# Kernel tuning notes

Hardware: AMD Instinct MI355X
Metric: run time of the kernel (lower is better)

## Reference

```python
import jax, jax.numpy as jnp
import numpy as np

B, C, L = 32, 512, 4096
H, K = 8, 3            # heads, kernel_size
D = C // H             # head dim
G = 32                 # GroupNorm groups
PAD = (K - 1) // 2
EPS = 1e-5
NEG = -1e30


def setup_inputs() -> dict:
    key = jax.random.key(0)
    ks = jax.random.split(key, 7)
    s = 0.02
    return {
        "x": jax.random.normal(ks[0], (B, C, L), dtype=jnp.float32),
        "gamma": jnp.ones((C,), dtype=jnp.float32),
        "beta": jnp.zeros((C,), dtype=jnp.float32),
        "W_k": jax.random.normal(ks[1], (C, H * D), dtype=jnp.float32) * s,
        "W_v": jax.random.normal(ks[2], (C, H * D), dtype=jnp.float32) * s,
        "W_o": jax.random.normal(ks[3], (H * D, C), dtype=jnp.float32) * s,
        "q": jax.random.normal(ks[4], (H, D), dtype=jnp.float32) * s,     # learned queries (QnA)
        "rpe": jax.random.normal(ks[5], (H, K), dtype=jnp.float32) * s,   # relative-position bias
    }


def _group_norm(x, gamma, beta):
    # x: (B, C, L); normalize over (C//G, L) within each of G groups
    b, c, l = x.shape
    xg = x.reshape(b, G, (c // G) * l)
    mu = jnp.mean(xg, axis=-1, keepdims=True)
    var = jnp.var(xg, axis=-1, keepdims=True)
    xn = ((xg - mu) * jax.lax.rsqrt(var + EPS)).reshape(b, c, l)
    return xn * gamma[None, :, None] + beta[None, :, None]


def reference(x, gamma, beta, W_k, W_v, W_o, q, rpe):
    h = _group_norm(x, gamma, beta)                     # (B, C, L)
    ht = jnp.transpose(h, (0, 2, 1))                    # (B, L, C)
    k = (ht @ W_k).reshape(B, L, H, D)                  # (B, L, H, D)
    v = (ht @ W_v).reshape(B, L, H, D)

    scale = 1.0 / np.sqrt(D).astype(np.float32)
    logits = jnp.einsum('blhd,hd->blh', k, q) * scale   # (B, L, H)

    # sliding windows of size K (zero-padded; -inf logits at boundaries)
    lp = jnp.pad(logits, ((0, 0), (PAD, PAD), (0, 0)), constant_values=NEG)
    lwin = jnp.stack([lp[:, j:j + L] for j in range(K)], axis=2)      # (B, L, K, H)
    lwin = lwin + jnp.transpose(rpe)[None, None]                       # rpe: (H,K)->(K,H)
    attn = jax.nn.softmax(lwin, axis=2)                                # (B, L, K, H)

    vp = jnp.pad(v, ((0, 0), (PAD, PAD), (0, 0), (0, 0)))
    vwin = jnp.stack([vp[:, j:j + L] for j in range(K)], axis=2)       # (B, L, K, H, D)
    o = jnp.einsum('blkh,blkhd->blhd', attn, vwin).reshape(B, L, H * D)

    out = (o @ W_o)                                      # (B, L, C)
    return x + jnp.transpose(out, (0, 2, 1))             # residual, (B, C, L)
```

## Files before the change

kernel.cpp:

```cpp
#include <hip/hip_runtime.h>

#define Bb 32
#define Cc 512
#define Ll 4096
#define Hh 8
#define Dd 64
#define Gg 32
#define BLt (Bb * Ll)
#define NKV 520
#define NKVPAD 640

typedef __attribute__((ext_vector_type(4))) float f32x4;
typedef __attribute__((ext_vector_type(8))) short short8;
typedef __attribute__((ext_vector_type(4))) short s16x4;
typedef __attribute__((ext_vector_type(4))) int int4v;

union U16 { int4v v; short s[8]; };

__device__ __forceinline__ float bf2f(short s) {
    unsigned u = ((unsigned)(unsigned short)s) << 16;
    float f; __builtin_memcpy(&f, &u, 4); return f;
}
__device__ __forceinline__ short f2bf(float f) {
    unsigned u; __builtin_memcpy(&u, &f, 4);
    u = (u + 0x7FFFu + ((u >> 16) & 1u)) >> 16;
    return (short)u;
}

__device__ __forceinline__ int kpack(int k) {
    int blk = k >> 5, r = k & 31;
    return blk * 32 + ((r & 15) >> 2) * 8 + ((r >> 4) << 2) + (r & 3);
}

__device__ __forceinline__ int swz_off(int row, int inner) {
    return row * 128 + (inner ^ ((row & 7) << 4));
}

__device__ __forceinline__ void gload16(const short* g, short* l) {
    __builtin_amdgcn_global_load_lds((const __attribute__((address_space(1))) unsigned int*)g,
                                     (__attribute__((address_space(3))) unsigned int*)l,
                                     16, 0, 0);
}

#define BAR() __builtin_amdgcn_s_barrier()
#define SFENCE() __builtin_amdgcn_sched_barrier(0)

__global__ void k_prep(const float* __restrict__ Wk, const float* __restrict__ Wv,
                       const float* __restrict__ Wo, const float* __restrict__ q,
                       short* __restrict__ Wct, short* __restrict__ Wot, int packWo)
{
    int bid = blockIdx.x, t = threadIdx.x;
    if (bid < NKVPAD) {
        int n = bid;
        if (n < 512) {
            for (int k = t; k < 512; k += 64)
                Wct[n * 512 + kpack(k)] = f2bf(Wv[k * 512 + n]);
        } else if (n < NKV) {
            int h = n - 512;
            for (int k = t; k < 512; k += 64) {
                float acc = 0.f;
                for (int d = 0; d < 64; ++d)
                    acc += Wk[k * 512 + h * 64 + d] * q[h * 64 + d];
                Wct[n * 512 + kpack(k)] = f2bf(acc * 0.125f);
            }
        } else {
            for (int k = t; k < 512; k += 64) Wct[n * 512 + kpack(k)] = 0;
        }
    } else {
        int c = bid - NKVPAD;
        for (int k = t; k < 512; k += 64)
            Wot[c * 512 + (packWo ? kpack(k) : k)] = f2bf(Wo[k * 512 + c]);
    }
}

__global__ void k_stats(const float* __restrict__ x, float* __restrict__ stats)
{
    int bg = blockIdx.x;
    const float* p = x + (size_t)bg * 65536;
    int t = threadIdx.x;
    float s = 0.f, ss = 0.f;
    for (int i = t * 4; i < 65536; i += 1024) {
        f32x4 v = *(const f32x4*)(p + i);
        s  += v[0] + v[1] + v[2] + v[3];
        ss += v[0]*v[0] + v[1]*v[1] + v[2]*v[2] + v[3]*v[3];
    }
    for (int o = 32; o > 0; o >>= 1) { s += __shfl_down(s, o); ss += __shfl_down(ss, o); }
    __shared__ float red[8];
    int lane = t & 63, w = t >> 6;
    if (lane == 0) { red[w] = s; red[4 + w] = ss; }
    __syncthreads();
    if (t == 0) {
        float S  = red[0] + red[1] + red[2] + red[3];
        float SS = red[4] + red[5] + red[6] + red[7];
        float mean = S * (1.0f / 65536.0f);
        float var  = SS * (1.0f / 65536.0f) - mean * mean;
        stats[bg * 2]     = mean;
        stats[bg * 2 + 1] = rsqrtf(var + 1e-5f);
    }
}

__global__ void k_norm_t(const float* __restrict__ x, const float* __restrict__ gamma,
                         const float* __restrict__ beta, const float* __restrict__ stats,
                         short* __restrict__ hT)
{
    __shared__ float tile[64 * 65];
    int b = blockIdx.z, c0 = blockIdx.y * 64, l0 = blockIdx.x * 64;
    int t = threadIdx.x;
    int lq = t & 15, cq = t >> 4;
    #pragma unroll
    for (int p = 0; p < 4; ++p) {
        int cl = cq + p * 16;
        int c = c0 + cl;
        float mean = stats[(b * 32 + (c >> 4)) * 2];
        float rstd = stats[(b * 32 + (c >> 4)) * 2 + 1];
        float a  = rstd * gamma[c];
        float bb = beta[c] - mean * a;
        f32x4 v = *(const f32x4*)(x + ((size_t)b << 21) + ((size_t)c << 12) + l0 + lq * 4);
        #pragma unroll
        for (int j = 0; j < 4; ++j) tile[cl * 65 + lq * 4 + j] = v[j] * a + bb;
    }
    __syncthreads();
    int ll = t >> 2, cq4 = t & 3;
    int bl = b * Ll + l0 + ll;
    short hbuf[16];
    #pragma unroll
    for (int j = 0; j < 16; ++j) hbuf[j] = f2bf(tile[(cq4 * 16 + j) * 65 + ll]);
    short* dst = hT + (size_t)bl * 512 + ((c0 >> 5) + (cq4 >> 1)) * 32 + ((cq4 & 1) << 2);
    #pragma unroll
    for (int jj = 0; jj < 4; ++jj) {
        s16x4 v4 = { hbuf[jj*4+0], hbuf[jj*4+1], hbuf[jj*4+2], hbuf[jj*4+3] };
        *(s16x4*)(dst + jj * 8) = v4;
    }
}


template<bool PACKED>
__launch_bounds__(256, 2)
__global__ void k_gemm1(const short* __restrict__ A, const short* __restrict__ Bw,
                        short* __restrict__ vbuf, short* __restrict__ lbuf)
{
    __shared__ short sA[2][8192];
    __shared__ short sB[2][8192];
    const int t = threadIdx.x;
    const int nwg = gridDim.x * gridDim.y;
    const int bid = blockIdx.x + gridDim.x * blockIdx.y;
    const int work = (bid & 7) * (nwg >> 3) + (bid >> 3);
    const int n0 = (work % gridDim.x) * 128;
    const int m0 = (work / gridDim.x) * 128;

    const int lane = t & 63, wid = t >> 6;
    const int wm = wid >> 1, wn = wid & 1;
    const int g = lane >> 4, ln = lane & 15;

    const int srow = wid * 8 + (lane >> 3);
    const int sinner = (((lane & 7) ^ ((lane >> 3) & 7)) << 3);
    const short* gAs = A  + (size_t)(m0 + srow) * 512 + sinner;
    const short* gBs = Bw + (size_t)(n0 + srow) * 512 + sinner;

    f32x4 acc[4][4] = {};

    auto stage = [&](int kt, int buf) {
        #pragma unroll
        for (int gq = 0; gq < 4; ++gq) {
            gload16(gAs + (size_t)gq * 32 * 512 + kt * 64, &sA[buf][gq * 2048 + wid * 512]);
            gload16(gBs + (size_t)gq * 32 * 512 + kt * 64, &sB[buf][gq * 2048 + wid * 512]);
        }
    };
    auto compute = [&](int buf) {
        #pragma unroll
        for (int ks = 0; ks < 2; ++ks) {
            short8 af[4], bfr[4];
            #pragma unroll
            for (int i = 0; i < 4; ++i) {
                af[i]  = *(const short8*)((const char*)&sA[buf][0] + swz_off(wm * 64 + i * 16 + ln, ks * 64 + g * 16));
                bfr[i] = *(const short8*)((const char*)&sB[buf][0] + swz_off(wn * 64 + i * 16 + ln, ks * 64 + g * 16));
            }
            #pragma unroll
            for (int mi = 0; mi < 4; ++mi)
                #pragma unroll
                for (int ni = 0; ni < 4; ++ni)
                    acc[mi][ni] = __builtin_amdgcn_mfma_f32_16x16x32_bf16(af[mi], bfr[ni], acc[mi][ni], 0, 0, 0);
        }
    };

    stage(0, 0); stage(1, 1);
    #pragma unroll 1
    for (int kt = 0; kt < 8; ++kt) {
        if (kt < 7) asm volatile("s_waitcnt vmcnt(8)" ::: "memory");
        else        asm volatile("s_waitcnt vmcnt(0)" ::: "memory");
        BAR(); SFENCE();
        compute(kt & 1);
        SFENCE();
        if (kt < 6) { BAR(); stage(kt + 2, kt & 1); }
    }

    if constexpr (PACKED) {
        if (n0 < 512) {
            BAR();
            short* scr = &sA[0][0] + wid * 4096;
            #pragma unroll
            for (int mi = 0; mi < 4; ++mi)
                #pragma unroll
                for (int ni = 0; ni < 4; ++ni)
                    #pragma unroll
                    for (int i = 0; i < 4; ++i)
                        scr[(mi * 16 + g * 4 + i) * 64 + ni * 16 + ln] = f2bf(acc[mi][ni][i]);
            asm volatile("s_waitcnt lgkmcnt(0)" ::: "memory");
            SFENCE();
            const int c8 = lane & 7, blkq = c8 >> 2, jq = c8 & 3;
            #pragma unroll
            for (int it = 0; it < 8; ++it) {
                int mrow = it * 8 + (lane >> 3);
                const short* bp = scr + mrow * 64 + blkq * 32;
                s16x4 lo = *(const s16x4*)(bp + 4 * jq);
                s16x4 hi = *(const s16x4*)(bp + 16 + 4 * jq);
                union { int4v v; s16x4 h[2]; } ov;
                ov.h[0] = lo; ov.h[1] = hi;
                int m = m0 + wm * 64 + mrow;
                int nc = n0 + wn * 64 + blkq * 32 + jq * 8;
                *(int4v*)(vbuf + (size_t)m * 512 + nc) = ov.v;
            }
        } else {
            #pragma unroll
            for (int mi = 0; mi < 4; ++mi)
                #pragma unroll
                for (int ni = 0; ni < 4; ++ni) {
                    int n = n0 + wn * 64 + ni * 16 + ln;
                    if (n >= 512 && n < NKV) {
                        #pragma unroll
                        for (int i = 0; i < 4; ++i) {
                            int m = m0 + wm * 64 + mi * 16 + g * 4 + i;
                            lbuf[(size_t)m * 8 + (n - 512)] = f2bf(acc[mi][ni][i]);
                        }
                    }
                }
        }
    } else {
        #pragma unroll
        for (int mi = 0; mi < 4; ++mi)
            #pragma unroll
            for (int ni = 0; ni < 4; ++ni) {
                int n = n0 + wn * 64 + ni * 16 + ln;
                if (n < NKV) {
                    #pragma unroll
                    for (int i = 0; i < 4; ++i) {
                        int m = m0 + wm * 64 + mi * 16 + g * 4 + i;
                        vbuf[(size_t)m * NKV + n] = f2bf(acc[mi][ni][i]);
                    }
                }
            }
    }
}

__global__ void k_combine(const short* __restrict__ vbuf, const short* __restrict__ lbuf,
                          const float* __restrict__ rpe, short* __restrict__ obuf)
{
    int t = threadIdx.x;
    int bl = blockIdx.x * 16 + (t >> 4);
    int blkd = t & 15;
    int h = blkd >> 1;
    int l = bl & (Ll - 1);
    int bm = (l == 0) ? bl : bl - 1;
    int bp = (l == Ll - 1) ? bl : bl + 1;
    float lg0 = (l > 0)      ? bf2f(lbuf[(size_t)bm * 8 + h]) + rpe[h * 3 + 0] : -1e30f;
    float lg1 =                bf2f(lbuf[(size_t)bl * 8 + h]) + rpe[h * 3 + 1];
    float lg2 = (l < Ll - 1) ? bf2f(lbuf[(size_t)bp * 8 + h]) + rpe[h * 3 + 2] : -1e30f;
    float m = fmaxf(lg1, fmaxf(lg0, lg2));
    float e0 = (l > 0)      ? __expf(lg0 - m) : 0.f;
    float e1 =                __expf(lg1 - m);
    float e2 = (l < Ll - 1) ? __expf(lg2 - m) : 0.f;
    float inv = 1.0f / (e0 + e1 + e2);
    float w0 = e0 * inv, w1 = e1 * inv, w2 = e2 * inv;

    const short8* vm = (const short8*)(vbuf + (size_t)bm * 512 + blkd * 32);
    const short8* v0 = (const short8*)(vbuf + (size_t)bl * 512 + blkd * 32);
    const short8* vp = (const short8*)(vbuf + (size_t)bp * 512 + blkd * 32);
    short8* dst = (short8*)(obuf + (size_t)bl * 512 + blkd * 32);
    #pragma unroll
    for (int qq = 0; qq < 4; ++qq) {
        short8 a = vm[qq], b = v0[qq], c = vp[qq], r;
        #pragma unroll
        for (int j = 0; j < 8; ++j)
            r[j] = f2bf(w0 * bf2f(a[j]) + w1 * bf2f(b[j]) + w2 * bf2f(c[j]));
        dst[qq] = r;
    }
}

__launch_bounds__(256, 2)
__global__ void k_gemm2p(const short* __restrict__ Wot, const short* __restrict__ obuf,
                         const float* __restrict__ x, float* __restrict__ out)
{
    __shared__ short sA[2][8192];
    __shared__ short sB[2][8192];
    const int t = threadIdx.x;
    const int nwg = gridDim.x * gridDim.y;
    const int bid = blockIdx.x + gridDim.x * blockIdx.y;
    const int work = (bid & 7) * (nwg >> 3) + (bid >> 3);
    const int m0 = (work % gridDim.x) * 128;
    const int n0 = (work / gridDim.x) * 128;

    const int lane = t & 63, wid = t >> 6;
    const int wm = wid >> 1, wn = wid & 1;
    const int g = lane >> 4, ln = lane & 15;

    const int srow = wid * 8 + (lane >> 3);
    const int sinner = (((lane & 7) ^ ((lane >> 3) & 7)) << 3);
    const short* gAs = Wot  + (size_t)(m0 + srow) * 512 + sinner;
    const short* gBs = obuf + (size_t)(n0 + srow) * 512 + sinner;

    f32x4 acc[4][4] = {};

    auto stage = [&](int kt, int buf) {
        #pragma unroll
        for (int gq = 0; gq < 4; ++gq) {
            gload16(gAs + (size_t)gq * 32 * 512 + kt * 64, &sA[buf][gq * 2048 + wid * 512]);
            gload16(gBs + (size_t)gq * 32 * 512 + kt * 64, &sB[buf][gq * 2048 + wid * 512]);
        }
    };
    auto compute = [&](int buf) {
        #pragma unroll
        for (int ks = 0; ks < 2; ++ks) {
            short8 af[4], bfr[4];
            #pragma unroll
            for (int i = 0; i < 4; ++i) {
                af[i]  = *(const short8*)((const char*)&sA[buf][0] + swz_off(wm * 64 + i * 16 + ln, ks * 64 + g * 16));
                bfr[i] = *(const short8*)((const char*)&sB[buf][0] + swz_off(wn * 64 + i * 16 + ln, ks * 64 + g * 16));
            }
            #pragma unroll
            for (int mi = 0; mi < 4; ++mi)
                #pragma unroll
                for (int ni = 0; ni < 4; ++ni)
                    acc[mi][ni] = __builtin_amdgcn_mfma_f32_16x16x32_bf16(af[mi], bfr[ni], acc[mi][ni], 0, 0, 0);
        }
    };

    stage(0, 0); stage(1, 1);
    #pragma unroll 1
    for (int kt = 0; kt < 8; ++kt) {
        if (kt < 7) asm volatile("s_waitcnt vmcnt(8)" ::: "memory");
        else        asm volatile("s_waitcnt vmcnt(0)" ::: "memory");
        BAR(); SFENCE();
        compute(kt & 1);
        SFENCE();
        if (kt < 6) { BAR(); stage(kt + 2, kt & 1); }
    }

    #pragma unroll
    for (int mi = 0; mi < 4; ++mi)
        #pragma unroll
        for (int ni = 0; ni < 4; ++ni)
            #pragma unroll
            for (int i = 0; i < 4; ++i) {
                int c = m0 + wm * 64 + mi * 16 + g * 4 + i;
                int ng = n0 + wn * 64 + ni * 16 + ln;
                int b = ng >> 12, l = ng & (Ll - 1);
                size_t off = ((size_t)b << 21) | ((size_t)c << 12) | (size_t)l;
                out[off] = x[off] + acc[mi][ni][i];
            }
}

__global__ void k_attnw(const short* __restrict__ kv, const float* __restrict__ rpe,
                        float* __restrict__ attnW)
{
    int tid = blockIdx.x * 256 + threadIdx.x;
    int bl = tid >> 3, h = tid & 7;
    int l = bl & (Ll - 1);
    float lg[3];
    #pragma unroll
    for (int j = 0; j < 3; ++j) {
        bool valid = (j == 1) || (j == 0 && l > 0) || (j == 2 && l < Ll - 1);
        lg[j] = valid ? (bf2f(kv[(size_t)(bl + j - 1) * NKV + 512 + h]) + rpe[h * 3 + j])
                      : -1e30f;
    }
    float m = fmaxf(lg[0], fmaxf(lg[1], lg[2]));
    float e0 = __expf(lg[0] - m), e1 = __expf(lg[1] - m), e2 = __expf(lg[2] - m);
    float inv = 1.0f / (e0 + e1 + e2);
    f32x4 w = { e0 * inv, e1 * inv, e2 * inv, 0.0f };
    *(f32x4*)(attnW + (size_t)bl * 32 + h * 4) = w;
}

__launch_bounds__(256, 2)
__global__ void k_gemm2_fused(const short* __restrict__ Wot, const short* __restrict__ kv,
                              const float* __restrict__ attnW, const float* __restrict__ x,
                              float* __restrict__ out)
{
    __shared__ short sA[2][8192];
    __shared__ short sB[2][8192];
    const int t = threadIdx.x;
    const int m0 = blockIdx.x * 128;
    const int n0 = blockIdx.y * 128;
    const int lane = t & 63, wid = t >> 6;
    const int wm = wid >> 1, wn = wid & 1;
    const int g = lane >> 4, ln = lane & 15;
    const int sr = t >> 1, ksh = t & 1;

    const short* gA = Wot + (size_t)(m0 + sr) * 512 + ksh * 32;
    const int nrow = n0 + sr;
    const int lpos = nrow & (Ll - 1);
    const int nm1 = (lpos == 0) ? nrow : nrow - 1;
    const int np1 = (lpos == Ll - 1) ? nrow : nrow + 1;
    const short* gV0 = kv + (size_t)nrow * NKV + ksh * 32;
    const short* gVm = kv + (size_t)nm1  * NKV + ksh * 32;
    const short* gVp = kv + (size_t)np1  * NKV + ksh * 32;
    const float* gW = attnW + (size_t)nrow * 32;

    f32x4 acc[4][4] = {};
    U16 ra[4], rbm[4], rb0[4], rbp[4];
    f32x4 wv;

    auto load_tile = [&](int kt) {
        #pragma unroll
        for (int qq = 0; qq < 4; ++qq) {
            ra[qq].v  = *(const int4v*)(gA  + kt * 64 + qq * 8);
            rbm[qq].v = *(const int4v*)(gVm + kt * 64 + qq * 8);
            rb0[qq].v = *(const int4v*)(gV0 + kt * 64 + qq * 8);
            rbp[qq].v = *(const int4v*)(gVp + kt * 64 + qq * 8);
        }
        wv = *(const f32x4*)(gW + kt * 4);
    };
    auto write_tile = [&](int buf) {
        short ob[32];
        #pragma unroll
        for (int qq = 0; qq < 4; ++qq)
            #pragma unroll
            for (int j = 0; j < 8; ++j) {
                float o = wv[0] * bf2f(rbm[qq].s[j]) + wv[1] * bf2f(rb0[qq].s[j])
                        + wv[2] * bf2f(rbp[qq].s[j]);
                ob[qq * 8 + j] = f2bf(o);
            }
        #pragma unroll
        for (int f = 0; f < 4; ++f) {
            U16 wa, wb;
            #pragma unroll
            for (int j = 0; j < 4; ++j) {
                wa.s[j]     = ra[f >> 1].s[(f & 1) * 4 + j];
                wa.s[4 + j] = ra[2 + (f >> 1)].s[(f & 1) * 4 + j];
                wb.s[j]     = ob[4 * f + j];
                wb.s[4 + j] = ob[16 + 4 * f + j];
            }
            int off = swz_off(sr, ksh * 64 + f * 16);
            *(int4v*)((char*)&sA[buf][0] + off) = wa.v;
            *(int4v*)((char*)&sB[buf][0] + off) = wb.v;
        }
    };
    auto compute = [&](int buf) {
        #pragma unroll
        for (int ks = 0; ks < 2; ++ks) {
            short8 af[4], bfr[4];
            #pragma unroll
            for (int i = 0; i < 4; ++i) {
                af[i]  = *(const short8*)((const char*)&sA[buf][0] + swz_off(wm * 64 + i * 16 + ln, ks * 64 + g * 16));
                bfr[i] = *(const short8*)((const char*)&sB[buf][0] + swz_off(wn * 64 + i * 16 + ln, ks * 64 + g * 16));
            }
            #pragma unroll
            for (int mi = 0; mi < 4; ++mi)
                #pragma unroll
                for (int ni = 0; ni < 4; ++ni)
                    acc[mi][ni] = __builtin_amdgcn_mfma_f32_16x16x32_bf16(af[mi], bfr[ni], acc[mi][ni], 0, 0, 0);
        }
    };

    load_tile(0); write_tile(0); __syncthreads();
    #pragma unroll 1
    for (int kt = 0; kt < 8; ++kt) {
        if (kt < 7) load_tile(kt + 1);
        compute(kt & 1);
        if (kt < 7) write_tile((kt + 1) & 1);
        __syncthreads();
    }

    #pragma unroll
    for (int mi = 0; mi < 4; ++mi)
        #pragma unroll
        for (int ni = 0; ni < 4; ++ni)
            #pragma unroll
            for (int i = 0; i < 4; ++i) {
                int c = m0 + wm * 64 + mi * 16 + g * 4 + i;
                int ng = n0 + wn * 64 + ni * 16 + ln;
                int b = ng >> 12, l = ng & (Ll - 1);
                size_t off = ((size_t)b << 21) | ((size_t)c << 12) | (size_t)l;
                out[off] = x[off] + acc[mi][ni][i];
            }
}

extern "C" void kernel_launch(void* const* d_in, const int* in_sizes, int n_in,
                              void* d_out, int out_size, void* d_ws, size_t ws_size,
                              hipStream_t stream)
{
    const float* x     = (const float*)d_in[0];
    const float* gamma = (const float*)d_in[1];
    const float* beta  = (const float*)d_in[2];
    const float* Wk    = (const float*)d_in[3];
    const float* Wv    = (const float*)d_in[4];
    const float* Wo    = (const float*)d_in[5];
    const float* q     = (const float*)d_in[6];
    const float* rpe   = (const float*)d_in[7];
    float* out = (float*)d_out;
    char* ws = (char*)d_ws;

    const size_t MB128 = 134217728ull;
    const size_t MAIN_WS = MB128 * 2 + 655360 + 524288 + 2097152 + 8192;

    if (ws_size >= MAIN_WS) {
        short* obuf  = (short*)(ws);
        short* vbuf  = (short*)(ws + MB128);
        short* Wct   = (short*)(ws + 2 * MB128);
        short* Wot   = (short*)(ws + 2 * MB128 + 655360);
        short* lbuf  = (short*)(ws + 2 * MB128 + 655360 + 524288);
        float* stats = (float*)(ws + 2 * MB128 + 655360 + 524288 + 2097152);
        short* hT    = (short*)d_out;

        k_prep<<<1152, 64, 0, stream>>>(Wk, Wv, Wo, q, Wct, Wot, 1);
        k_stats<<<1024, 256, 0, stream>>>(x, stats);
        k_norm_t<<<dim3(64, 8, 32), 256, 0, stream>>>(x, gamma, beta, stats, hT);
        k_gemm1<true><<<dim3(5, 1024), 256, 0, stream>>>(hT, Wct, vbuf, lbuf);
        k_combine<<<8192, 256, 0, stream>>>(vbuf, lbuf, rpe, obuf);
        k_gemm2p<<<dim3(4, 1024), 256, 0, stream>>>(Wot, obuf, x, out);
    } else {
        short* Wct   = (short*)(ws + 0);
        short* Wot   = (short*)(ws + 655360);
        float* stats = (float*)(ws + 1179648);
        float* attnW = (float*)(ws + 1187840);
        short* kv    = (short*)(ws + 17965056);
        short* hT    = (short*)d_out;

        k_prep<<<1152, 64, 0, stream>>>(Wk, Wv, Wo, q, Wct, Wot, 0);
        k_stats<<<1024, 256, 0, stream>>>(x, stats);
        k_norm_t<<<dim3(64, 8, 32), 256, 0, stream>>>(x, gamma, beta, stats, hT);
        k_gemm1<false><<<dim3(5, 1024), 256, 0, stream>>>(hT, Wct, kv, nullptr);
        k_attnw<<<4096, 256, 0, stream>>>(kv, rpe, attnW);
        k_gemm2_fused<<<dim3(4, 1024), 256, 0, stream>>>(Wot, kv, attnW, x, out);
    }
}
```

Baseline: 542.4 us.

## Make GEMM kernels persistent over multiple M tiles with continuous pipelining

Both main-path GEMMs now have each workgroup walk four 128-row tiles in sequence, running 32 k-steps in one continuous pipeline. The prologue and epilogue bubbles are paid once per four tiles instead of once per tile. The streamed operand gets a triple buffer with a two-to-three stage prefetch distance, and each tile's accumulators are written out, then zeroed at tile boundaries. Grids shrink to 1280 and 1024 workgroups, which means fewer waves and more LDS per block, and this may lower occupancy. The fallback path gets a simpler separate GEMM kernel.

```diff
diff --git a/kernel.cpp b/kernel.cpp
--- a/kernel.cpp
+++ b/kernel.cpp
@@ -134,19 +134,18 @@
 }
 
 
-template<bool PACKED>
 __launch_bounds__(256, 2)
-__global__ void k_gemm1(const short* __restrict__ A, const short* __restrict__ Bw,
-                        short* __restrict__ vbuf, short* __restrict__ lbuf)
-{
-    __shared__ short sA[2][8192];
+__global__ void k_gemm1f(const short* __restrict__ A, const short* __restrict__ Bw,
+                         short* __restrict__ vbuf, short* __restrict__ lbuf)
+{
+    __shared__ short sA[3][8192];
     __shared__ short sB[2][8192];
     const int t = threadIdx.x;
-    const int nwg = gridDim.x * gridDim.y;
-    const int bid = blockIdx.x + gridDim.x * blockIdx.y;
+    const int nwg = 1280;
+    const int bid = blockIdx.x;
     const int work = (bid & 7) * (nwg >> 3) + (bid >> 3);
-    const int n0 = (work % gridDim.x) * 128;
-    const int m0 = (work / gridDim.x) * 128;
+    const int n0 = (work % 5) * 128;
+    const int mbase = (work / 5) * 512;
 
     const int lane = t & 63, wid = t >> 6;
     const int wm = wid >> 1, wn = wid & 1;
@@ -154,26 +153,31 @@
 
     const int srow = wid * 8 + (lane >> 3);
     const int sinner = (((lane & 7) ^ ((lane >> 3) & 7)) << 3);
-    const short* gAs = A  + (size_t)(m0 + srow) * 512 + sinner;
+    const short* gAs = A  + (size_t)(mbase + srow) * 512 + sinner;
     const short* gBs = Bw + (size_t)(n0 + srow) * 512 + sinner;
 
     f32x4 acc[4][4] = {};
 
-    auto stage = [&](int kt, int buf) {
-        #pragma unroll
-        for (int gq = 0; gq < 4; ++gq) {
-            gload16(gAs + (size_t)gq * 32 * 512 + kt * 64, &sA[buf][gq * 2048 + wid * 512]);
-            gload16(gBs + (size_t)gq * 32 * 512 + kt * 64, &sB[buf][gq * 2048 + wid * 512]);
-        }
-    };
-    auto compute = [&](int buf) {
+    auto stageA = [&](int s, int buf) {
+        size_t off = (size_t)(s >> 3) * 65536 + (size_t)(s & 7) * 64;
+        #pragma unroll
+        for (int gq = 0; gq < 4; ++gq)
+            gload16(gAs + (size_t)gq * 32 * 512 + off, &sA[buf][gq * 2048 + wid * 512]);
+    };
+    auto stageB = [&](int s, int buf) {
+        size_t off = (size_t)(s & 7) * 64;
+        #pragma unroll
+        for (int gq = 0; gq < 4; ++gq)
+            gload16(gBs + (size_t)gq * 32 * 512 + off, &sB[buf][gq * 2048 + wid * 512]);
+    };
+    auto compute = [&](int ab, int bb) {
         #pragma unroll
         for (int ks = 0; ks < 2; ++ks) {
             short8 af[4], bfr[4];
             #pragma unroll
             for (int i = 0; i < 4; ++i) {
-                af[i]  = *(const short8*)((const char*)&sA[buf][0] + swz_off(wm * 64 + i * 16 + ln, ks * 64 + g * 16));
-                bfr[i] = *(const short8*)((const char*)&sB[buf][0] + swz_off(wn * 64 + i * 16 + ln, ks * 64 + g * 16));
+                af[i]  = *(const short8*)((const char*)&sA[ab][0] + swz_off(wm * 64 + i * 16 + ln, ks * 64 + g * 16));
+                bfr[i] = *(const short8*)((const char*)&sB[bb][0] + swz_off(wn * 64 + i * 16 + ln, ks * 64 + g * 16));
             }
             #pragma unroll
             for (int mi = 0; mi < 4; ++mi)
@@ -183,72 +187,67 @@
         }
     };
 
-    stage(0, 0); stage(1, 1);
+    stageB(0, 0); stageB(1, 1); stageA(0, 0); stageA(1, 1); stageA(2, 2);
     #pragma unroll 1
-    for (int kt = 0; kt < 8; ++kt) {
-        if (kt < 7) asm volatile("s_waitcnt vmcnt(8)" ::: "memory");
-        else        asm volatile("s_waitcnt vmcnt(0)" ::: "memory");
+    for (int s = 0; s < 32; ++s) {
+        if (s == 31)              asm volatile("s_waitcnt vmcnt(0)"  ::: "memory");
+        else if (s == 0 || s == 30) asm volatile("s_waitcnt vmcnt(8)"  ::: "memory");
+        else                      asm volatile("s_waitcnt vmcnt(12)" ::: "memory");
         BAR(); SFENCE();
-        compute(kt & 1);
+        compute(s % 3, s & 1);
         SFENCE();
-        if (kt < 6) { BAR(); stage(kt + 2, kt & 1); }
-    }
-
-    if constexpr (PACKED) {
-        if (n0 < 512) {
+        if ((s & 7) == 7) {
             BAR();
-            short* scr = &sA[0][0] + wid * 4096;
-            #pragma unroll
-            for (int mi = 0; mi < 4; ++mi)
-                #pragma unroll
-                for (int ni = 0; ni < 4; ++ni)
+            int m0 = mbase + (s >> 3) * 128;
+            if (n0 < 512) {
+                short* scrW = &sB[s & 1][0] + wid * 2048;
+                const int blkq = (lane & 7) >> 2, jq = lane & 3;
+                #pragma unroll
+                for (int p = 0; p < 2; ++p) {
                     #pragma unroll
-                    for (int i = 0; i < 4; ++i)
-                        scr[(mi * 16 + g * 4 + i) * 64 + ni * 16 + ln] = f2bf(acc[mi][ni][i]);
-            asm volatile("s_waitcnt lgkmcnt(0)" ::: "memory");
-            SFENCE();
-            const int c8 = lane & 7, blkq = c8 >> 2, jq = c8 & 3;
-            #pragma unroll
-            for (int it = 0; it < 8; ++it) {
-                int mrow = it * 8 + (lane >> 3);
-                const short* bp = scr + mrow * 64 + blkq * 32;
-                s16x4 lo = *(const s16x4*)(bp + 4 * jq);
-                s16x4 hi = *(const s16x4*)(bp + 16 + 4 * jq);
-                union { int4v v; s16x4 h[2]; } ov;
-                ov.h[0] = lo; ov.h[1] = hi;
-                int m = m0 + wm * 64 + mrow;
-                int nc = n0 + wn * 64 + blkq * 32 + jq * 8;
-                *(int4v*)(vbuf + (size_t)m * 512 + nc) = ov.v;
-            }
-        } else {
-            #pragma unroll
-            for (int mi = 0; mi < 4; ++mi)
-                #pragma unroll
-                for (int ni = 0; ni < 4; ++ni) {
-                    int n = n0 + wn * 64 + ni * 16 + ln;
-                    if (n >= 512 && n < NKV) {
+                    for (int mh = 0; mh < 2; ++mh)
+                        #pragma unroll
+                        for (int ni = 0; ni < 4; ++ni)
+                            #pragma unroll
+                            for (int i = 0; i < 4; ++i)
+                                scrW[(mh * 16 + g * 4 + i) * 64 + ni * 16 + ln] = f2bf(acc[p * 2 + mh][ni][i]);
+                    asm volatile("s_waitcnt lgkmcnt(0)" ::: "memory"); SFENCE();
+                    #pragma unroll
+                    for (int it = 0; it < 4; ++it) {
+                        int mrl = it * 8 + (lane >> 3);
+                        const short* bp = scrW + mrl * 64 + blkq * 32;
+                        s16x4 lo = *(const s16x4*)(bp + 4 * jq);
+                        s16x4 hi = *(const s16x4*)(bp + 16 + 4 * jq);
+                        union { int4v v; s16x4 h[2]; } ov;
+                        ov.h[0] = lo; ov.h[1] = hi;
+                        int m = m0 + wm * 64 + p * 32 + mrl;
+                        int nc = n0 + wn * 64 + blkq * 32 + jq * 8;
+                        *(int4v*)(vbuf + (size_t)m * 512 + nc) = ov.v;
+                    }
+                    asm volatile("s_waitcnt lgkmcnt(0)" ::: "memory"); SFENCE();
+                }
+            } else {
+                if (wn == 0 && ln < 8) {
+                    #pragma unroll
+                    for (int mi = 0; mi < 4; ++mi)
                         #pragma unroll
                         for (int i = 0; i < 4; ++i) {
                             int m = m0 + wm * 64 + mi * 16 + g * 4 + i;
-                            lbuf[(size_t)m * 8 + (n - 512)] = f2bf(acc[mi][ni][i]);
+                            lbuf[(size_t)m * 8 + ln] = f2bf(acc[mi][0][i]);
                         }
-                    }
                 }
-        }
-    } else {
-        #pragma unroll
-        for (int mi = 0; mi < 4; ++mi)
-            #pragma unroll
-            for (int ni = 0; ni < 4; ++ni) {
-                int n = n0 + wn * 64 + ni * 16 + ln;
-                if (n < NKV) {
-                    #pragma unroll
-                    for (int i = 0; i < 4; ++i) {
-                        int m = m0 + wm * 64 + mi * 16 + g * 4 + i;
-                        vbuf[(size_t)m * NKV + n] = f2bf(acc[mi][ni][i]);
-                    }
-                }
-            }
+            }
+            #pragma unroll
+            for (int mi = 0; mi < 4; ++mi)
+                #pragma unroll
+                for (int ni = 0; ni < 4; ++ni)
+                    acc[mi][ni] = (f32x4){0.f, 0.f, 0.f, 0.f};
+        }
+        if (s < 30) {
+            BAR();
+            stageB(s + 2, s & 1);
+            if (s < 29) stageA(s + 3, (s + 3) % 3);
+        }
     }
 }
 
@@ -287,26 +286,111 @@
 }
 
 __launch_bounds__(256, 2)
-__global__ void k_gemm2p(const short* __restrict__ Wot, const short* __restrict__ obuf,
+__global__ void k_gemm2f(const short* __restrict__ Wot, const short* __restrict__ obuf,
                          const float* __restrict__ x, float* __restrict__ out)
+{
+    __shared__ short sA[2][8192];
+    __shared__ short sB[3][8192];
+    const int t = threadIdx.x;
+    const int nwg = 1024;
+    const int bid = blockIdx.x;
+    const int work = (bid & 7) * (nwg >> 3) + (bid >> 3);
+    const int n0 = work * 128;
+
+    const int lane = t & 63, wid = t >> 6;
+    const int wm = wid >> 1, wn = wid & 1;
+    const int g = lane >> 4, ln = lane & 15;
+
+    const int srow = wid * 8 + (lane >> 3);
+    const int sinner = (((lane & 7) ^ ((lane >> 3) & 7)) << 3);
+    const short* gAs = Wot  + (size_t)srow * 512 + sinner;
+    const short* gBs = obuf + (size_t)(n0 + srow) * 512 + sinner;
+
+    f32x4 acc[4][4] = {};
+
+    auto stageA = [&](int s, int buf) {
+        size_t off = (size_t)(s >> 3) * 65536 + (size_t)(s & 7) * 64;
+        #pragma unroll
+        for (int gq = 0; gq < 4; ++gq)
+            gload16(gAs + (size_t)gq * 32 * 512 + off, &sA[buf][gq * 2048 + wid * 512]);
+    };
+    auto stageB = [&](int s, int buf) {
+        size_t off = (size_t)(s & 7) * 64;
+        #pragma unroll
+        for (int gq = 0; gq < 4; ++gq)
+            gload16(gBs + (size_t)gq * 32 * 512 + off, &sB[buf][gq * 2048 + wid * 512]);
+    };
+    auto compute = [&](int ab, int bb) {
+        #pragma unroll
+        for (int ks = 0; ks < 2; ++ks) {
+            short8 af[4], bfr[4];
+            #pragma unroll
+            for (int i = 0; i < 4; ++i) {
+                af[i]  = *(const short8*)((const char*)&sA[ab][0] + swz_off(wm * 64 + i * 16 + ln, ks * 64 + g * 16));
+                bfr[i] = *(const short8*)((const char*)&sB[bb][0] + swz_off(wn * 64 + i * 16 + ln, ks * 64 + g * 16));
+            }
+            #pragma unroll
+            for (int mi = 0; mi < 4; ++mi)
+                #pragma unroll
+                for (int ni = 0; ni < 4; ++ni)
+                    acc[mi][ni] = __builtin_amdgcn_mfma_f32_16x16x32_bf16(af[mi], bfr[ni], acc[mi][ni], 0, 0, 0);
+        }
+    };
+
+    stageA(0, 0); stageA(1, 1); stageB(0, 0); stageB(1, 1); stageB(2, 2);
+    #pragma unroll 1
+    for (int s = 0; s < 32; ++s) {
+        if (s == 31)              asm volatile("s_waitcnt vmcnt(0)"  ::: "memory");
+        else if (s == 0 || s == 30) asm volatile("s_waitcnt vmcnt(8)"  ::: "memory");
+        else                      asm volatile("s_waitcnt vmcnt(12)" ::: "memory");
+        BAR(); SFENCE();
+        compute(s & 1, s % 3);
+        SFENCE();
+        if ((s & 7) == 7) {
+            int m0c = (s >> 3) * 128;
+            #pragma unroll
+            for (int mi = 0; mi < 4; ++mi)
+                #pragma unroll
+                for (int ni = 0; ni < 4; ++ni)
+                    #pragma unroll
+                    for (int i = 0; i < 4; ++i) {
+                        int c = m0c + wm * 64 + mi * 16 + g * 4 + i;
+                        int ng = n0 + wn * 64 + ni * 16 + ln;
+                        int b = ng >> 12, l = ng & (Ll - 1);
+                        size_t off = ((size_t)b << 21) | ((size_t)c << 12) | (size_t)l;
+                        out[off] = x[off] + acc[mi][ni][i];
+                    }
+            #pragma unroll
+            for (int mi = 0; mi < 4; ++mi)
+                #pragma unroll
+                for (int ni = 0; ni < 4; ++ni)
+                    acc[mi][ni] = (f32x4){0.f, 0.f, 0.f, 0.f};
+        }
+        if (s < 30) {
+            BAR();
+            stageA(s + 2, s & 1);
+            if (s < 29) stageB(s + 3, (s + 3) % 3);
+        }
+    }
+}
+
+__launch_bounds__(256, 2)
+__global__ void k_gemm1_fb(const short* __restrict__ A, const short* __restrict__ Bw,
+                           short* __restrict__ kv)
 {
     __shared__ short sA[2][8192];
     __shared__ short sB[2][8192];
     const int t = threadIdx.x;
-    const int nwg = gridDim.x * gridDim.y;
-    const int bid = blockIdx.x + gridDim.x * blockIdx.y;
-    const int work = (bid & 7) * (nwg >> 3) + (bid >> 3);
-    const int m0 = (work % gridDim.x) * 128;
-    const int n0 = (work / gridDim.x) * 128;
-
+    const int m0 = blockIdx.y * 128;
+    const int n0 = blockIdx.x * 128;
     const int lane = t & 63, wid = t >> 6;
     const int wm = wid >> 1, wn = wid & 1;
     const int g = lane >> 4, ln = lane & 15;
 
     const int srow = wid * 8 + (lane >> 3);
     const int sinner = (((lane & 7) ^ ((lane >> 3) & 7)) << 3);
-    const short* gAs = Wot  + (size_t)(m0 + srow) * 512 + sinner;
-    const short* gBs = obuf + (size_t)(n0 + srow) * 512 + sinner;
+    const short* gAs = A  + (size_t)(m0 + srow) * 512 + sinner;
+    const short* gBs = Bw + (size_t)(n0 + srow) * 512 + sinner;
 
     f32x4 acc[4][4] = {};
 
@@ -334,29 +418,28 @@
         }
     };
 
-    stage(0, 0); stage(1, 1);
+    stage(0, 0);
+    __syncthreads();
     #pragma unroll 1
     for (int kt = 0; kt < 8; ++kt) {
-        if (kt < 7) asm volatile("s_waitcnt vmcnt(8)" ::: "memory");
-        else        asm volatile("s_waitcnt vmcnt(0)" ::: "memory");
-        BAR(); SFENCE();
+        if (kt < 7) stage(kt + 1, (kt + 1) & 1);
         compute(kt & 1);
-        SFENCE();
-        if (kt < 6) { BAR(); stage(kt + 2, kt & 1); }
+        __syncthreads();
     }
 
     #pragma unroll
     for (int mi = 0; mi < 4; ++mi)
         #pragma unroll
-        for (int ni = 0; ni < 4; ++ni)
-            #pragma unroll
-            for (int i = 0; i < 4; ++i) {
-                int c = m0 + wm * 64 + mi * 16 + g * 4 + i;
-                int ng = n0 + wn * 64 + ni * 16 + ln;
-                int b = ng >> 12, l = ng & (Ll - 1);
-                size_t off = ((size_t)b << 21) | ((size_t)c << 12) | (size_t)l;
-                out[off] = x[off] + acc[mi][ni][i];
-            }
+        for (int ni = 0; ni < 4; ++ni) {
+            int n = n0 + wn * 64 + ni * 16 + ln;
+            if (n < NKV) {
+                #pragma unroll
+                for (int i = 0; i < 4; ++i) {
+                    int m = m0 + wm * 64 + mi * 16 + g * 4 + i;
+                    kv[(size_t)m * NKV + n] = f2bf(acc[mi][ni][i]);
+                }
+            }
+        }
 }
 
 __global__ void k_attnw(const short* __restrict__ kv, const float* __restrict__ rpe,
@@ -513,9 +596,9 @@
         k_prep<<<1152, 64, 0, stream>>>(Wk, Wv, Wo, q, Wct, Wot, 1);
         k_stats<<<1024, 256, 0, stream>>>(x, stats);
         k_norm_t<<<dim3(64, 8, 32), 256, 0, stream>>>(x, gamma, beta, stats, hT);
-        k_gemm1<true><<<dim3(5, 1024), 256, 0, stream>>>(hT, Wct, vbuf, lbuf);
+        k_gemm1f<<<1280, 256, 0, stream>>>(hT, Wct, vbuf, lbuf);
         k_combine<<<8192, 256, 0, stream>>>(vbuf, lbuf, rpe, obuf);
-        k_gemm2p<<<dim3(4, 1024), 256, 0, stream>>>(Wot, obuf, x, out);
+        k_gemm2f<<<1024, 256, 0, stream>>>(Wot, obuf, x, out);
     } else {
         short* Wct   = (short*)(ws + 0);
         short* Wot   = (short*)(ws + 655360);
@@ -527,7 +610,7 @@
         k_prep<<<1152, 64, 0, stream>>>(Wk, Wv, Wo, q, Wct, Wot, 0);
         k_stats<<<1024, 256, 0, stream>>>(x, stats);
         k_norm_t<<<dim3(64, 8, 32), 256, 0, stream>>>(x, gamma, beta, stats, hT);
-        k_gemm1<false><<<dim3(5, 1024), 256, 0, stream>>>(hT, Wct, kv, nullptr);
+        k_gemm1_fb<<<dim3(5, 1024), 256, 0, stream>>>(hT, Wct, kv);
         k_attnw<<<4096, 256, 0, stream>>>(kv, rpe, attnW);
         k_gemm2_fused<<<dim3(4, 1024), 256, 0, stream>>>(Wot, kv, attnW, x, out);
     }
```

New measurement: 555.0 us. 1.02x slower.
